# Optimization experiments

Hardware: AMD Instinct MI355X
Metric: run time of the kernel (lower is better)

## Reference

```python
import jax, jax.numpy as jnp
import numpy as np

N = 20000      # nodes (all graphs in batch)
E = 320000     # edges (avg degree 16)
G = 16         # graphs in batch
D_IN = 32      # raw node feature dim
D_LAP = 16     # laplacian PE dim
D = 256        # d_model
H = 8          # heads
DH = D // H    # head dim
L = 2          # encoder layers
D_FF = 2 * D   # FFN hidden (FFN_layer1: d_model -> 2*d_model)
EPS = 1e-5


def _layer_norm(x, g, b):
    m = jnp.mean(x, axis=-1, keepdims=True)
    v = jnp.var(x, axis=-1, keepdims=True)
    return g * (x - m) * jax.lax.rsqrt(v + EPS) + b


def setup_inputs() -> dict:
    key = jax.random.key(0)
    ks = jax.random.split(key, 32)

    feat = jax.random.normal(ks[0], (N, D_IN), dtype=jnp.float32)
    lap_pos = jax.random.normal(ks[1], (N, D_LAP), dtype=jnp.float32)
    # random +-1 sign flip per PE dim (done with torch.rand in the original forward)
    sign_flip = jnp.where(jax.random.uniform(ks[2], (D_LAP,)) >= 0.5, 1.0, -1.0).astype(jnp.float32)

    src = jax.random.randint(ks[3], (E,), 0, N, dtype=jnp.int32)
    dst = jax.random.randint(ks[4], (E,), 0, N, dtype=jnp.int32)
    graph_ids = jnp.sort(jax.random.randint(ks[5], (N,), 0, G, dtype=jnp.int32))

    def xavier(k, shape):
        fan_in, fan_out = shape[-2], shape[-1]
        lim = np.sqrt(6.0 / (fan_in + fan_out))
        return jax.random.uniform(k, shape, minval=-lim, maxval=lim, dtype=jnp.float32)

    inp = {
        "feat": feat, "lap_pos": lap_pos, "sign_flip": sign_flip,
        "src": src, "dst": dst, "graph_ids": graph_ids,
        # input embeddings
        "Wh": xavier(ks[6], (D_IN, D)), "bh": jnp.zeros((D,), jnp.float32),
        "Wlp": xavier(ks[7], (D_LAP, D)), "blp": jnp.zeros((D,), jnp.float32),
        # per-layer params, stacked on leading layer axis
        "Wq": xavier(ks[8], (L, D, D)), "Wk": xavier(ks[9], (L, D, D)),
        "Wv": xavier(ks[10], (L, D, D)),
        "Wo": xavier(ks[11], (L, D, D)), "bo": jnp.zeros((L, D), jnp.float32),
        "g1": jnp.ones((L, D), jnp.float32), "b1": jnp.zeros((L, D), jnp.float32),
        "W1": xavier(ks[12], (L, D, D_FF)), "c1": jnp.zeros((L, D_FF), jnp.float32),
        "W2": xavier(ks[13], (L, D_FF, D)), "c2": jnp.zeros((L, D), jnp.float32),
        "g2": jnp.ones((L, D), jnp.float32), "b2": jnp.zeros((L, D), jnp.float32),
    }
    return inp


def _forward(feat, lap_pos, sign_flip, src, dst, graph_ids,
             Wh, bh, Wlp, blp, Wq, Wk, Wv, Wo, bo, g1, b1, W1, c1, W2, c2, g2, b2):
    scale = np.sqrt(DH).astype(np.float32)

    h = feat @ Wh + bh                                  # [N, D]
    h = h + (lap_pos * sign_flip[None, :]) @ Wlp + blp  # add PE embedding

    for l in range(L):
        h_in1 = h
        Q = (h @ Wq[l]).reshape(N, H, DH)
        K = (h @ Wk[l]).reshape(N, H, DH)
        V = (h @ Wv[l]).reshape(N, H, DH)

        # per-edge dot-product score, then exp(clamp(score/sqrt(dh), -5, 5))
        score = jnp.sum(K[src] * Q[dst], axis=-1)                       # [E, H]
        s = jnp.exp(jnp.clip(score / scale, -5.0, 5.0))                # [E, H]

        # segment softmax of s over incoming edges per dst node (F.softmax on mailbox)
        m = jax.ops.segment_max(s, dst, num_segments=N)                 # [N, H], -inf if no in-edges
        p = jnp.exp(s - m[dst])                                         # [E, H]
        den = jax.ops.segment_sum(p, dst, num_segments=N)               # [N, H]
        msg = jax.ops.segment_sum(p[:, :, None] * V[src], dst, num_segments=N)  # [N, H, DH]
        attn = msg / jnp.where(den > 0, den, 1.0)[:, :, None]
        attn = attn.reshape(N, D)

        h = _layer_norm(h_in1 + attn @ Wo[l] + bo[l], g1[l], b1[l])
        h_in2 = h
        ff = jax.nn.relu(h @ W1[l] + c1[l]) @ W2[l] + c2[l]
        h = _layer_norm(h_in2 + ff, g2[l], b2[l])

    # mean readout per graph
    counts = jax.ops.segment_sum(jnp.ones((N,), h.dtype), graph_ids, num_segments=G)
    sums = jax.ops.segment_sum(h, graph_ids, num_segments=G)            # [G, D]
    return sums / jnp.where(counts > 0, counts, 1.0)[:, None]


def reference(feat, lap_pos, sign_flip, src, dst, graph_ids,
              Wh, bh, Wlp, blp, Wq, Wk, Wv, Wo, bo, g1, b1, W1, c1, W2, c2, g2, b2):
    return _forward(feat, lap_pos, sign_flip, src, dst, graph_ids,
                    Wh, bh, Wlp, blp, Wq, Wk, Wv, Wo, bo, g1, b1, W1, c1, W2, c2, g2, b2)
```

## Files before the change

### kernel.cpp

```cpp
#include <hip/hip_runtime.h>
#include <hip/hip_bf16.h>

#define NN   20000
#define EE   320000
#define GG   16
#define DD   256
#define HH   8
#define DHH  32
#define LLAYERS 2
#define DFF  512
#define DIN  32
#define DLAP 16
#define RSPLITS 16

typedef __attribute__((ext_vector_type(8))) short bf16x8;
typedef __attribute__((ext_vector_type(8))) unsigned short u16x8;
typedef __attribute__((ext_vector_type(4))) float f32x4;

__device__ __forceinline__ void gld_lds16(const void* g, void* l) {
  __builtin_amdgcn_global_load_lds((const __attribute__((address_space(1))) uint32_t*)g,
                                   (__attribute__((address_space(3))) uint32_t*)l, 16, 0, 0);
}

__device__ __forceinline__ float b2f(unsigned short s) {
  union { unsigned int i; float f; } u;
  u.i = ((unsigned int)s) << 16;
  return u.f;
}

__device__ __forceinline__ unsigned short f2bu(float f) {
  __hip_bfloat16 b = __float2bfloat16(f);
  return *(unsigned short*)&b;
}

__global__ __launch_bounds__(256) void k_embed(
    const float* __restrict__ feat, const float* __restrict__ lap,
    const float* __restrict__ sign, const float* __restrict__ Wh,
    const float* __restrict__ bh, const float* __restrict__ Wlp,
    const float* __restrict__ blp, float* __restrict__ h,
    __hip_bfloat16* __restrict__ hb) {
  int n = blockIdx.x;
  int d = threadIdx.x;
  float acc = bh[d] + blp[d];
  const float* frow = feat + (size_t)n * DIN;
  const float* lrow = lap + (size_t)n * DLAP;
#pragma unroll
  for (int k = 0; k < DIN; ++k) acc += frow[k] * Wh[k * DD + d];
#pragma unroll
  for (int k = 0; k < DLAP; ++k) acc += (lrow[k] * sign[k]) * Wlp[k * DD + d];
  h[(size_t)n * DD + d] = acc;
  hb[(size_t)n * DD + d] = __float2bfloat16(acc);
}

__global__ __launch_bounds__(256) void k_wt_all(
    const float* __restrict__ Wq, const float* __restrict__ Wk,
    const float* __restrict__ Wv, const float* __restrict__ Wo,
    const float* __restrict__ W1, const float* __restrict__ W2,
    __hip_bfloat16* __restrict__ Wqt, __hip_bfloat16* __restrict__ Wkt,
    __hip_bfloat16* __restrict__ Wvt, __hip_bfloat16* __restrict__ Wot,
    __hip_bfloat16* __restrict__ W1t, __hip_bfloat16* __restrict__ W2t) {
  __shared__ float tile[32][33];
  int z = blockIdx.z;
  const float* in;
  __hip_bfloat16* out;
  int K, N, l;
  if (z < 8) {
    int widx = z >> 1;
    l = z & 1;
    K = DD; N = DD;
    in = (widx == 0) ? Wq : (widx == 1) ? Wk : (widx == 2) ? Wv : Wo;
    out = (widx == 0) ? Wqt : (widx == 1) ? Wkt : (widx == 2) ? Wvt : Wot;
  } else if (z < 10) {
    l = z - 8; K = DD; N = DFF; in = W1; out = W1t;
  } else {
    l = z - 10; K = DFF; N = DD; in = W2; out = W2t;
  }
  int bx = blockIdx.x, by = blockIdx.y;
  if (bx * 32 >= N || by * 32 >= K) return;
  const float* inl = in + (size_t)l * K * N;
  __hip_bfloat16* outl = out + (size_t)l * N * K;
  int tx = threadIdx.x & 31, ty = threadIdx.x >> 5;
#pragma unroll
  for (int i = 0; i < 32; i += 8)
    tile[ty + i][tx] = inl[(size_t)(by * 32 + ty + i) * N + bx * 32 + tx];
  __syncthreads();
#pragma unroll
  for (int i = 0; i < 32; i += 8)
    outl[(size_t)(bx * 32 + ty + i) * K + by * 32 + tx] = __float2bfloat16(tile[tx][ty + i]);
}

template <bool BIAS, bool RELU, bool KVPACK>
__global__ __launch_bounds__(256) void gemm_mfma(
    const __hip_bfloat16* __restrict__ A,
    const __hip_bfloat16* __restrict__ Bt0, const __hip_bfloat16* __restrict__ Bt1,
    const __hip_bfloat16* __restrict__ Bt2,
    const float* __restrict__ bias,
    __hip_bfloat16* __restrict__ C0, __hip_bfloat16* __restrict__ C1,
    int M, int K, int ldc0) {
  const __hip_bfloat16* Bt = (blockIdx.z == 0) ? Bt0 : (blockIdx.z == 1) ? Bt1 : Bt2;
  __hip_bfloat16* Cout = (blockIdx.z == 0) ? C0 : C1;
  const int vo = (blockIdx.z == 2) ? 4 : 0;

  __shared__ short lA[2][4][128][8];
  __shared__ short lB[2][4][128][8];

  const int t = threadIdx.x;
  const int lane = t & 63, w = t >> 6;
  const int bm = blockIdx.x * 128, bn = blockIdx.y * 128;
  const int wr = w >> 1, wc = w & 1;
  const int fr = lane & 15, fg = lane >> 4;

  f32x4 acc[4][4] = {};

  auto stage = [&](int buf, int kt) {
    const int k0 = kt * 32;
#pragma unroll
    for (int it = 0; it < 2; ++it) {
      const int cbase = it * 256 + w * 64;
      const int c = cbase + lane;
      const int g = c >> 7, r = c & 127;
      int arow = bm + r;
      if (arow >= M) arow = M - 1;
      gld_lds16(A + (size_t)arow * K + k0 + g * 8,
                (short*)lA + ((size_t)buf * 512 + cbase) * 8);
      gld_lds16(Bt + (size_t)(bn + r) * K + k0 + g * 8,
                (short*)lB + ((size_t)buf * 512 + cbase) * 8);
    }
  };

  const int nt = K >> 5;
  stage(0, 0);
  for (int kt = 0; kt < nt; ++kt) {
    const int buf = kt & 1;
    __syncthreads();
    if (kt + 1 < nt) stage(buf ^ 1, kt + 1);
    bf16x8 af[4], bfr[4];
#pragma unroll
    for (int i = 0; i < 4; ++i)
      af[i] = *(const bf16x8*)&lA[buf][fg][wr * 64 + i * 16 + fr][0];
#pragma unroll
    for (int j = 0; j < 4; ++j)
      bfr[j] = *(const bf16x8*)&lB[buf][fg][wc * 64 + j * 16 + fr][0];
#pragma unroll
    for (int i = 0; i < 4; ++i)
#pragma unroll
      for (int j = 0; j < 4; ++j)
        acc[i][j] = __builtin_amdgcn_mfma_f32_16x16x32_bf16(af[i], bfr[j], acc[i][j], 0, 0, 0);
  }

#pragma unroll
  for (int i = 0; i < 4; ++i) {
    const int row0 = bm + wr * 64 + i * 16 + fg * 4;
#pragma unroll
    for (int j = 0; j < 4; ++j) {
      const int col = bn + wc * 64 + j * 16 + fr;
      float bv = BIAS ? bias[col] : 0.f;
#pragma unroll
      for (int r = 0; r < 4; ++r) {
        const int row = row0 + r;
        if (row >= M) continue;
        float v = acc[i][j][r] + bv;
        if (RELU) v = fmaxf(v, 0.f);
        if (KVPACK && blockIdx.z != 0) {
          Cout[(size_t)row * (2 * DD) + ((col >> 2) << 3) + vo + (col & 3)] =
              __float2bfloat16(v);
        } else {
          Cout[(size_t)row * ldc0 + col] = __float2bfloat16(v);
        }
      }
    }
  }
}

template <int KK>
__global__ __launch_bounds__(256) void gemm_ln(
    const __hip_bfloat16* __restrict__ A,
    const __hip_bfloat16* __restrict__ Bt,
    const float* __restrict__ bias,
    float* __restrict__ h,
    __hip_bfloat16* __restrict__ hb,
    const float* __restrict__ g, const float* __restrict__ b,
    int M) {
  __shared__ float redS[16];
  __shared__ float redQ[16];

  const int t = threadIdx.x;
  const int lane = t & 63, w = t >> 6;
  const int bm = blockIdx.x * 16;
  const int fr = lane & 15, fg = lane >> 4;

  if (t < 16) { redS[t] = 0.f; redQ[t] = 0.f; }

  f32x4 acc[4] = {};
  const __hip_bfloat16* ap = A + (size_t)(bm + fr) * KK + fg * 8;
  const __hip_bfloat16* bp = Bt + (size_t)(w * 64 + fr) * KK + fg * 8;

#pragma unroll 4
  for (int kt = 0; kt < KK / 32; ++kt) {
    const int k0 = kt * 32;
    bf16x8 af = *(const bf16x8*)(ap + k0);
    bf16x8 bfr[4];
#pragma unroll
    for (int j = 0; j < 4; ++j)
      bfr[j] = *(const bf16x8*)(bp + (size_t)j * 16 * KK + k0);
#pragma unroll
    for (int j = 0; j < 4; ++j)
      acc[j] = __builtin_amdgcn_mfma_f32_16x16x32_bf16(af, bfr[j], acc[j], 0, 0, 0);
  }

  __syncthreads();
#pragma unroll
  for (int r = 0; r < 4; ++r) {
    const int lrow = fg * 4 + r;
    const int grow = bm + lrow;
    float s = 0.f, q = 0.f;
#pragma unroll
    for (int j = 0; j < 4; ++j) {
      const int col = w * 64 + j * 16 + fr;
      float x = acc[j][r] + bias[col] + h[(size_t)grow * DD + col];
      acc[j][r] = x;
      s += x;
      q += x * x;
    }
#pragma unroll
    for (int o = 1; o < 16; o <<= 1) {
      s += __shfl_xor(s, o);
      q += __shfl_xor(q, o);
    }
    if (fr == 0) {
      atomicAdd(&redS[lrow], s);
      atomicAdd(&redQ[lrow], q);
    }
  }
  __syncthreads();
#pragma unroll
  for (int r = 0; r < 4; ++r) {
    const int lrow = fg * 4 + r;
    const int grow = bm + lrow;
    const float mean = redS[lrow] * (1.f / 256.f);
    const float var = redQ[lrow] * (1.f / 256.f) - mean * mean;
    const float rs = rsqrtf(var + 1e-5f);
#pragma unroll
    for (int j = 0; j < 4; ++j) {
      const int col = w * 64 + j * 16 + fr;
      float v = g[col] * ((acc[j][r] - mean) * rs) + b[col];
      h[(size_t)grow * DD + col] = v;
      hb[(size_t)grow * DD + col] = __float2bfloat16(v);
    }
  }
}

__global__ void k_hist(const int* __restrict__ dst, int* __restrict__ deg, int n) {
  int i = blockIdx.x * blockDim.x + threadIdx.x;
  if (i < n) atomicAdd(&deg[dst[i]], 1);
}

__global__ __launch_bounds__(256) void k_scan_block(
    const int* __restrict__ in, int* __restrict__ ex, int* __restrict__ bsum, int n) {
  __shared__ int sm[256];
  int t = threadIdx.x;
  int i = blockIdx.x * 256 + t;
  int v = (i < n) ? in[i] : 0;
  sm[t] = v;
  __syncthreads();
  for (int o = 1; o < 256; o <<= 1) {
    int x = (t >= o) ? sm[t - o] : 0;
    __syncthreads();
    sm[t] += x;
    __syncthreads();
  }
  if (i < n) ex[i] = sm[t] - v;
  if (t == 255) bsum[blockIdx.x] = sm[255];
}

__global__ __launch_bounds__(256) void k_scan_top(
    const int* __restrict__ bsum, int* __restrict__ boff, int nb) {
  __shared__ int sm[256];
  int t = threadIdx.x;
  int v = (t < nb) ? bsum[t] : 0;
  sm[t] = v;
  __syncthreads();
  for (int o = 1; o < 256; o <<= 1) {
    int x = (t >= o) ? sm[t - o] : 0;
    __syncthreads();
    sm[t] += x;
    __syncthreads();
  }
  if (t < nb) boff[t] = sm[t] - v;
}

__global__ void k_finish_indptr(const int* __restrict__ ex, const int* __restrict__ boff,
                                int* __restrict__ indptr, int* __restrict__ cursor,
                                int n, int total) {
  int i = blockIdx.x * 256 + threadIdx.x;
  if (i < n) {
    int v = ex[i] + boff[i >> 8];
    indptr[i] = v;
    cursor[i] = v;
  }
  if (i == 0) indptr[n] = total;
}

__global__ void k_fill(const int* __restrict__ dst, const int* __restrict__ src,
                       int* __restrict__ cursor, int* __restrict__ csr_src, int n) {
  int i = blockIdx.x * blockDim.x + threadIdx.x;
  if (i < n) {
    int pos = atomicAdd(&cursor[dst[i]], 1);
    csr_src[pos] = src[i];
  }
}

__global__ void k_bounds(const int* __restrict__ gid, int* __restrict__ gb, int n) {
  int i = blockIdx.x * blockDim.x + threadIdx.x;
  if (i >= n) return;
  int g = gid[i];
  if (i == 0) {
    for (int x = 0; x <= g; ++x) gb[x] = 0;
  } else {
    int pg = gid[i - 1];
    for (int x = pg + 1; x <= g; ++x) gb[x] = i;
  }
  if (i == n - 1) {
    for (int x = g + 1; x <= GG; ++x) gb[x] = n;
  }
}

__global__ __launch_bounds__(256) void k_attn(
    const int* __restrict__ indptr, const int* __restrict__ csr_src,
    const __hip_bfloat16* __restrict__ Q, const __hip_bfloat16* __restrict__ kvb,
    __hip_bfloat16* __restrict__ attn) {
  int n = blockIdx.x * 4 + (threadIdx.x >> 6);
  if (n >= NN) return;
  int lane = threadIdx.x & 63;
  int half = lane >> 5;
  int sl = lane & 31;
  int doff = sl * 8;
  int s0 = indptr[n], s1 = indptr[n + 1];

  u16x8 qv = *(const u16x8*)((const unsigned short*)Q + (size_t)n * DD + doff);
  float q[8];
#pragma unroll
  for (int i = 0; i < 8; ++i) q[i] = b2f((unsigned short)qv[i]);

  const unsigned short* kvp = (const unsigned short*)kvb;

  float m = 0.f, den = 0.f;
  float a[8] = {};
  int j = s0 + half;
  if (j < s1) {
    const unsigned short* row = kvp + (size_t)csr_src[j] * (2 * DD) + sl * 16;
    u16x8 c0 = *(const u16x8*)row;
    u16x8 c1 = *(const u16x8*)(row + 8);
    for (; j < s1; j += 2) {
      int jn = (j + 2 < s1) ? j + 2 : j;
      const unsigned short* rown = kvp + (size_t)csr_src[jn] * (2 * DD) + sl * 16;
      u16x8 n0 = *(const u16x8*)rown;
      u16x8 n1 = *(const u16x8*)(rown + 8);

      float dot = q[0] * b2f((unsigned short)c0[0]) + q[1] * b2f((unsigned short)c0[1]) +
                  q[2] * b2f((unsigned short)c0[2]) + q[3] * b2f((unsigned short)c0[3]) +
                  q[4] * b2f((unsigned short)c1[0]) + q[5] * b2f((unsigned short)c1[1]) +
                  q[6] * b2f((unsigned short)c1[2]) + q[7] * b2f((unsigned short)c1[3]);
      dot += __shfl_xor(dot, 1);
      dot += __shfl_xor(dot, 2);
      float x = fminf(fmaxf(dot * 0.17677669529663687f, -5.f), 5.f);
      float s = __expf(x);
      if (s - m > 8.f) {
        float r = __expf(m - s);
        den *= r;
#pragma unroll
        for (int i = 0; i < 8; ++i) a[i] *= r;
        m = s;
      }
      float p = __expf(s - m);
      den += p;
      a[0] += p * b2f((unsigned short)c0[4]);
      a[1] += p * b2f((unsigned short)c0[5]);
      a[2] += p * b2f((unsigned short)c0[6]);
      a[3] += p * b2f((unsigned short)c0[7]);
      a[4] += p * b2f((unsigned short)c1[4]);
      a[5] += p * b2f((unsigned short)c1[5]);
      a[6] += p * b2f((unsigned short)c1[6]);
      a[7] += p * b2f((unsigned short)c1[7]);
      c0 = n0;
      c1 = n1;
    }
  }

  float mo = __shfl_xor(m, 32);
  float M = fmaxf(m, mo);
  float r = __expf(m - M);
  den *= r;
#pragma unroll
  for (int i = 0; i < 8; ++i) a[i] *= r;
  den += __shfl_xor(den, 32);
#pragma unroll
  for (int i = 0; i < 8; ++i) a[i] += __shfl_xor(a[i], 32);

  if (half == 0) {
    float inv = 1.f / (den > 0.f ? den : 1.f);
    u16x8 o;
#pragma unroll
    for (int i = 0; i < 8; ++i) o[i] = f2bu(a[i] * inv);
    *(u16x8*)((unsigned short*)attn + (size_t)n * DD + doff) = o;
  }
}

__global__ __launch_bounds__(256) void k_gmean(
    const float* __restrict__ h, const int* __restrict__ gb,
    float* __restrict__ gsum) {
  int g = blockIdx.x, s = blockIdx.y;
  int t = threadIdx.x;
  int r0 = gb[g], r1 = gb[g + 1];
  int len = r1 - r0;
  int per = (len + RSPLITS - 1) / RSPLITS;
  int a = r0 + s * per;
  int b = min(r1, a + per);
  if (a >= b) return;
  float acc = 0.f;
  for (int r = a; r < b; ++r) acc += h[(size_t)r * DD + t];
  atomicAdd(&gsum[g * DD + t], acc);
}

__global__ void k_final(const float* __restrict__ gsum, const int* __restrict__ gb,
                        float* __restrict__ out) {
  int g = blockIdx.x, t = threadIdx.x;
  int len = gb[g + 1] - gb[g];
  out[g * DD + t] = gsum[g * DD + t] / (len > 0 ? (float)len : 1.f);
}

extern "C" void kernel_launch(void* const* d_in, const int* in_sizes, int n_in,
                              void* d_out, int out_size, void* d_ws, size_t ws_size,
                              hipStream_t stream) {
  const float* feat = (const float*)d_in[0];
  const float* lap  = (const float*)d_in[1];
  const float* sign = (const float*)d_in[2];
  const int* srcs   = (const int*)d_in[3];
  const int* dsts   = (const int*)d_in[4];
  const int* gids   = (const int*)d_in[5];
  const float* Wh   = (const float*)d_in[6];
  const float* bh   = (const float*)d_in[7];
  const float* Wlp  = (const float*)d_in[8];
  const float* blp  = (const float*)d_in[9];
  const float* Wq   = (const float*)d_in[10];
  const float* Wk   = (const float*)d_in[11];
  const float* Wv   = (const float*)d_in[12];
  const float* Wo   = (const float*)d_in[13];
  const float* bo   = (const float*)d_in[14];
  const float* g1   = (const float*)d_in[15];
  const float* b1   = (const float*)d_in[16];
  const float* W1   = (const float*)d_in[17];
  const float* c1   = (const float*)d_in[18];
  const float* W2   = (const float*)d_in[19];
  const float* c2   = (const float*)d_in[20];
  const float* g2   = (const float*)d_in[21];
  const float* b2   = (const float*)d_in[22];

  char* base = (char*)d_ws;
  size_t off = 0;
  auto take = [&](size_t bytes) -> void* {
    void* p = base + off;
    off += (bytes + 255) & ~(size_t)255;
    return p;
  };
  float* h      = (float*)take((size_t)NN * DD * 4);
  __hip_bfloat16* hb  = (__hip_bfloat16*)take((size_t)NN * DD * 2);
  __hip_bfloat16* Qb  = (__hip_bfloat16*)take((size_t)NN * DD * 2);
  __hip_bfloat16* kvb = (__hip_bfloat16*)take((size_t)NN * 2 * DD * 2);
  __hip_bfloat16* t1b = (__hip_bfloat16*)take((size_t)NN * DFF * 2);
  __hip_bfloat16* Wqt = (__hip_bfloat16*)take((size_t)LLAYERS * DD * DD * 2);
  __hip_bfloat16* Wkt = (__hip_bfloat16*)take((size_t)LLAYERS * DD * DD * 2);
  __hip_bfloat16* Wvt = (__hip_bfloat16*)take((size_t)LLAYERS * DD * DD * 2);
  __hip_bfloat16* Wot = (__hip_bfloat16*)take((size_t)LLAYERS * DD * DD * 2);
  __hip_bfloat16* W1t = (__hip_bfloat16*)take((size_t)LLAYERS * DD * DFF * 2);
  __hip_bfloat16* W2t = (__hip_bfloat16*)take((size_t)LLAYERS * DFF * DD * 2);
  int* deg     = (int*)take((size_t)NN * 4);
  int* ex      = (int*)take((size_t)NN * 4);
  int* bsum    = (int*)take(256 * 4);
  int* boff    = (int*)take(256 * 4);
  int* indptr  = (int*)take((size_t)(NN + 1) * 4);
  int* cursor  = (int*)take((size_t)NN * 4);
  int* csr_src = (int*)take((size_t)EE * 4);
  int* gb      = (int*)take((size_t)(GG + 1) * 4);
  float* gsum  = (float*)take((size_t)GG * DD * 4);
  __hip_bfloat16* attnb = Qb;

  const int NB = (NN + 255) / 256;

  k_wt_all<<<dim3(DFF / 32, DFF / 32, 12), 256, 0, stream>>>(
      Wq, Wk, Wv, Wo, W1, W2, Wqt, Wkt, Wvt, Wot, W1t, W2t);

  hipMemsetAsync(deg, 0, (size_t)NN * 4, stream);
  k_hist<<<(EE + 255) / 256, 256, 0, stream>>>(dsts, deg, EE);
  k_scan_block<<<NB, 256, 0, stream>>>(deg, ex, bsum, NN);
  k_scan_top<<<1, 256, 0, stream>>>(bsum, boff, NB);
  k_finish_indptr<<<NB, 256, 0, stream>>>(ex, boff, indptr, cursor, NN, EE);
  k_fill<<<(EE + 255) / 256, 256, 0, stream>>>(dsts, srcs, cursor, csr_src, EE);
  k_bounds<<<NB, 256, 0, stream>>>(gids, gb, NN);

  k_embed<<<NN, 256, 0, stream>>>(feat, lap, sign, Wh, bh, Wlp, blp, h, hb);

  const int MB = (NN + 127) / 128;
  const int MB16 = (NN + 15) / 16;
  dim3 gQKV(MB, DD / 128, 3);
  dim3 gF(MB, DFF / 128, 1);

  for (int l = 0; l < LLAYERS; ++l) {
    const __hip_bfloat16* Wqt_l = Wqt + (size_t)l * DD * DD;
    const __hip_bfloat16* Wkt_l = Wkt + (size_t)l * DD * DD;
    const __hip_bfloat16* Wvt_l = Wvt + (size_t)l * DD * DD;
    const __hip_bfloat16* Wot_l = Wot + (size_t)l * DD * DD;
    const __hip_bfloat16* W1t_l = W1t + (size_t)l * DD * DFF;
    const __hip_bfloat16* W2t_l = W2t + (size_t)l * DFF * DD;
    const float* bo_l = bo + (size_t)l * DD;
    const float* g1_l = g1 + (size_t)l * DD;
    const float* b1_l = b1 + (size_t)l * DD;
    const float* c1_l = c1 + (size_t)l * DFF;
    const float* c2_l = c2 + (size_t)l * DD;
    const float* g2_l = g2 + (size_t)l * DD;
    const float* b2_l = b2 + (size_t)l * DD;

    gemm_mfma<false, false, true><<<gQKV, 256, 0, stream>>>(
        hb, Wqt_l, Wkt_l, Wvt_l, nullptr, Qb, kvb, NN, DD, DD);

    k_attn<<<(NN + 3) / 4, 256, 0, stream>>>(indptr, csr_src, Qb, kvb, attnb);

    gemm_ln<DD><<<MB16, 256, 0, stream>>>(attnb, Wot_l, bo_l, h, hb, g1_l, b1_l, NN);

    gemm_mfma<true, true, false><<<gF, 256, 0, stream>>>(
        hb, W1t_l, W1t_l, W1t_l, c1_l, t1b, t1b, NN, DD, DFF);

    gemm_ln<DFF><<<MB16, 256, 0, stream>>>(t1b, W2t_l, c2_l, h, hb, g2_l, b2_l, NN);
  }

  hipMemsetAsync(gsum, 0, (size_t)GG * DD * 4, stream);
  k_gmean<<<dim3(GG, RSPLITS), 256, 0, stream>>>(h, gb, gsum);
  k_final<<<GG, 256, 0, stream>>>(gsum, gb, (float*)d_out);
}
```

Before: 486.7 us.

## Split fused GEMM+LayerNorm into tiled MFMA GEMM plus separate LN kernel

Replaces the gemm_ln kernel, a 16-row-per-block GEMM with no LDS staging that is fused with the residual add and layer norm, by two kernels. The first is the tiled LDS double-buffered 128x128 gemm_mfma writing fp32 to a temporary buffer, and the second is a wave-per-row residual+LayerNorm kernel. The goal is better data reuse and MFMA efficiency in the Wo and W2 GEMMs, which previously reloaded B from global for every small row tile. The cost is an extra fp32 N×D round trip through memory and two extra launches per layer.

```diff
diff --git a/kernel.cpp b/kernel.cpp
--- a/kernel.cpp
+++ b/kernel.cpp
@@ -89,16 +89,16 @@
     outl[(size_t)(bx * 32 + ty + i) * K + by * 32 + tx] = __float2bfloat16(tile[tx][ty + i]);
 }
 
-template <bool BIAS, bool RELU, bool KVPACK>
+template <bool BIAS, bool RELU, bool KVPACK, bool OUTF32>
 __global__ __launch_bounds__(256) void gemm_mfma(
     const __hip_bfloat16* __restrict__ A,
     const __hip_bfloat16* __restrict__ Bt0, const __hip_bfloat16* __restrict__ Bt1,
     const __hip_bfloat16* __restrict__ Bt2,
     const float* __restrict__ bias,
-    __hip_bfloat16* __restrict__ C0, __hip_bfloat16* __restrict__ C1,
+    void* __restrict__ C0, void* __restrict__ C1,
     int M, int K, int ldc0) {
   const __hip_bfloat16* Bt = (blockIdx.z == 0) ? Bt0 : (blockIdx.z == 1) ? Bt1 : Bt2;
-  __hip_bfloat16* Cout = (blockIdx.z == 0) ? C0 : C1;
+  void* Cout = (blockIdx.z == 0) ? C0 : C1;
   const int vo = (blockIdx.z == 2) ? 4 : 0;
 
   __shared__ short lA[2][4][128][8];
@@ -162,91 +162,52 @@
         float v = acc[i][j][r] + bv;
         if (RELU) v = fmaxf(v, 0.f);
         if (KVPACK && blockIdx.z != 0) {
-          Cout[(size_t)row * (2 * DD) + ((col >> 2) << 3) + vo + (col & 3)] =
+          ((__hip_bfloat16*)Cout)[(size_t)row * (2 * DD) + ((col >> 2) << 3) + vo + (col & 3)] =
               __float2bfloat16(v);
+        } else if (OUTF32) {
+          ((float*)Cout)[(size_t)row * ldc0 + col] = v;
         } else {
-          Cout[(size_t)row * ldc0 + col] = __float2bfloat16(v);
+          ((__hip_bfloat16*)Cout)[(size_t)row * ldc0 + col] = __float2bfloat16(v);
         }
       }
     }
   }
 }
 
-template <int KK>
-__global__ __launch_bounds__(256) void gemm_ln(
-    const __hip_bfloat16* __restrict__ A,
-    const __hip_bfloat16* __restrict__ Bt,
-    const float* __restrict__ bias,
-    float* __restrict__ h,
-    __hip_bfloat16* __restrict__ hb,
+__global__ __launch_bounds__(256) void k_ln(
+    float* __restrict__ h, const float* __restrict__ add,
     const float* __restrict__ g, const float* __restrict__ b,
-    int M) {
-  __shared__ float redS[16];
-  __shared__ float redQ[16];
-
-  const int t = threadIdx.x;
-  const int lane = t & 63, w = t >> 6;
-  const int bm = blockIdx.x * 16;
-  const int fr = lane & 15, fg = lane >> 4;
-
-  if (t < 16) { redS[t] = 0.f; redQ[t] = 0.f; }
-
-  f32x4 acc[4] = {};
-  const __hip_bfloat16* ap = A + (size_t)(bm + fr) * KK + fg * 8;
-  const __hip_bfloat16* bp = Bt + (size_t)(w * 64 + fr) * KK + fg * 8;
-
-#pragma unroll 4
-  for (int kt = 0; kt < KK / 32; ++kt) {
-    const int k0 = kt * 32;
-    bf16x8 af = *(const bf16x8*)(ap + k0);
-    bf16x8 bfr[4];
-#pragma unroll
-    for (int j = 0; j < 4; ++j)
-      bfr[j] = *(const bf16x8*)(bp + (size_t)j * 16 * KK + k0);
-#pragma unroll
-    for (int j = 0; j < 4; ++j)
-      acc[j] = __builtin_amdgcn_mfma_f32_16x16x32_bf16(af, bfr[j], acc[j], 0, 0, 0);
-  }
-
-  __syncthreads();
-#pragma unroll
-  for (int r = 0; r < 4; ++r) {
-    const int lrow = fg * 4 + r;
-    const int grow = bm + lrow;
-    float s = 0.f, q = 0.f;
-#pragma unroll
-    for (int j = 0; j < 4; ++j) {
-      const int col = w * 64 + j * 16 + fr;
-      float x = acc[j][r] + bias[col] + h[(size_t)grow * DD + col];
-      acc[j][r] = x;
-      s += x;
-      q += x * x;
-    }
-#pragma unroll
-    for (int o = 1; o < 16; o <<= 1) {
-      s += __shfl_xor(s, o);
-      q += __shfl_xor(q, o);
-    }
-    if (fr == 0) {
-      atomicAdd(&redS[lrow], s);
-      atomicAdd(&redQ[lrow], q);
-    }
-  }
-  __syncthreads();
-#pragma unroll
-  for (int r = 0; r < 4; ++r) {
-    const int lrow = fg * 4 + r;
-    const int grow = bm + lrow;
-    const float mean = redS[lrow] * (1.f / 256.f);
-    const float var = redQ[lrow] * (1.f / 256.f) - mean * mean;
-    const float rs = rsqrtf(var + 1e-5f);
-#pragma unroll
-    for (int j = 0; j < 4; ++j) {
-      const int col = w * 64 + j * 16 + fr;
-      float v = g[col] * ((acc[j][r] - mean) * rs) + b[col];
-      h[(size_t)grow * DD + col] = v;
-      hb[(size_t)grow * DD + col] = __float2bfloat16(v);
-    }
+    __hip_bfloat16* __restrict__ hb, int n) {
+  int row = blockIdx.x * 4 + (threadIdx.x >> 6);
+  int lane = threadIdx.x & 63;
+  if (row >= n) return;
+  const size_t base = (size_t)row * DD;
+  float x[4];
+  float s = 0.f;
+#pragma unroll
+  for (int j = 0; j < 4; ++j) {
+    int d = lane + j * 64;
+    x[j] = h[base + d] + add[base + d];
+    s += x[j];
+  }
+#pragma unroll
+  for (int o = 32; o > 0; o >>= 1) s += __shfl_xor(s, o, 64);
+  float mean = s * (1.f / 256.f);
+  float vs = 0.f;
+#pragma unroll
+  for (int j = 0; j < 4; ++j) {
+    float d = x[j] - mean;
+    vs += d * d;
+  }
+#pragma unroll
+  for (int o = 32; o > 0; o >>= 1) vs += __shfl_xor(vs, o, 64);
+  float rs = rsqrtf(vs * (1.f / 256.f) + 1e-5f);
+#pragma unroll
+  for (int j = 0; j < 4; ++j) {
+    int d = lane + j * 64;
+    float v = g[d] * ((x[j] - mean) * rs) + b[d];
+    h[base + d] = v;
+    hb[base + d] = __float2bfloat16(v);
   }
 }
 
@@ -464,6 +425,7 @@
     return p;
   };
   float* h      = (float*)take((size_t)NN * DD * 4);
+  float* tmp    = (float*)take((size_t)NN * DD * 4);
   __hip_bfloat16* hb  = (__hip_bfloat16*)take((size_t)NN * DD * 2);
   __hip_bfloat16* Qb  = (__hip_bfloat16*)take((size_t)NN * DD * 2);
   __hip_bfloat16* kvb = (__hip_bfloat16*)take((size_t)NN * 2 * DD * 2);
@@ -501,8 +463,8 @@
   k_embed<<<NN, 256, 0, stream>>>(feat, lap, sign, Wh, bh, Wlp, blp, h, hb);
 
   const int MB = (NN + 127) / 128;
-  const int MB16 = (NN + 15) / 16;
   dim3 gQKV(MB, DD / 128, 3);
+  dim3 gD(MB, DD / 128, 1);
   dim3 gF(MB, DFF / 128, 1);
 
   for (int l = 0; l < LLAYERS; ++l) {
@@ -520,17 +482,20 @@
     const float* g2_l = g2 + (size_t)l * DD;
     const float* b2_l = b2 + (size_t)l * DD;
 
-    gemm_mfma<false, false, true><<<gQKV, 256, 0, stream>>>(
+    gemm_mfma<false, false, true, false><<<gQKV, 256, 0, stream>>>(
         hb, Wqt_l, Wkt_l, Wvt_l, nullptr, Qb, kvb, NN, DD, DD);
 
     k_attn<<<(NN + 3) / 4, 256, 0, stream>>>(indptr, csr_src, Qb, kvb, attnb);
 
-    gemm_ln<DD><<<MB16, 256, 0, stream>>>(attnb, Wot_l, bo_l, h, hb, g1_l, b1_l, NN);
-
-    gemm_mfma<true, true, false><<<gF, 256, 0, stream>>>(
+    gemm_mfma<true, false, false, true><<<gD, 256, 0, stream>>>(
+        attnb, Wot_l, Wot_l, Wot_l, bo_l, tmp, tmp, NN, DD, DD);
+    k_ln<<<NN / 4, 256, 0, stream>>>(h, tmp, g1_l, b1_l, hb, NN);
+
+    gemm_mfma<true, true, false, false><<<gF, 256, 0, stream>>>(
         hb, W1t_l, W1t_l, W1t_l, c1_l, t1b, t1b, NN, DD, DFF);
-
-    gemm_ln<DFF><<<MB16, 256, 0, stream>>>(t1b, W2t_l, c2_l, h, hb, g2_l, b2_l, NN);
+    gemm_mfma<true, false, false, true><<<gD, 256, 0, stream>>>(
+        t1b, W2t_l, W2t_l, W2t_l, c2_l, tmp, tmp, NN, DFF, DD);
+    k_ln<<<NN / 4, 256, 0, stream>>>(h, tmp, g2_l, b2_l, hb, NN);
   }
 
   hipMemsetAsync(gsum, 0, (size_t)GG * DD * 4, stream);
```

New measurement: 464.0 us. -4.7%, faster.
